# Kernel tuning notes

Measured on AMD Instinct MI355X. Metric: run time of the kernel, lower is better.

Reference implementation:

```python
import jax, jax.numpy as jnp
import numpy as np
from jax.scipy.linalg import solve_triangular

L_SUB = 16          # subarray length (init arg L)
DL = 0.05           # diagonal loading factor


def setup_inputs() -> dict:
    key = jax.random.key(0)
    k0, k1, k2 = jax.random.split(key, 3)
    B, C, NS, NZ, NX = 2, 128, 1024, 256, 128
    rf = jax.random.normal(k0, (B, C, NS), jnp.float32)
    t0 = jnp.zeros((B,), jnp.float32)
    d_tx = jax.random.uniform(k1, (B, NZ, NX), dtype=jnp.float32)
    d_rx = jax.random.uniform(k2, (C, NZ, NX), dtype=jnp.float32)
    fs = jnp.float32((NS - 1) / 2.0)   # keeps sample positions in [0, NS-1]
    f0 = jnp.float32(5.0)              # unused by forward (kept for signature parity)
    c0 = jnp.float32(1.0)
    apod = jnp.ones((C,), jnp.float32) # unused by forward
    return dict(rf=rf, t0=t0, d_tx=d_tx, d_rx=d_rx, fs=fs, f0=f0, c0=c0, apod=apod)


def _aligned_signals(rf, t0, d_tx, d_rx, fs, c0):
    """Bilinear (1-D linear) resample of rf at per-pixel delays.
    Equivalent to torch grid_sample(mode='bilinear', padding_mode='border',
    align_corners=True) where the grid x-coord is samples*2/(NS-1)-1."""
    B, C, NS = rf.shape
    _, NZ, NX = d_tx.shape
    # samples: [B, C, NZ, NX] fractional sample index into rf
    samples = fs * ((d_tx[:, None, :, :] + d_rx[None, :, :, :]) / c0
                    + t0[:, None, None, None])
    pos = jnp.clip(samples, 0.0, NS - 1.0)          # border padding
    i0 = jnp.floor(pos).astype(jnp.int32)
    i1 = jnp.minimum(i0 + 1, NS - 1)
    frac = pos - i0.astype(pos.dtype)
    sig = rf.reshape(B * C, NS)
    i0f = i0.reshape(B * C, NZ * NX)
    i1f = i1.reshape(B * C, NZ * NX)
    v0 = jnp.take_along_axis(sig, i0f, axis=1).reshape(B, C, NZ, NX)
    v1 = jnp.take_along_axis(sig, i1f, axis=1).reshape(B, C, NZ, NX)
    return v0 * (1.0 - frac) + v1 * frac


def reference(rf, t0, d_tx, d_rx, fs, f0, c0, apod):
    B, C, NS = rf.shape
    _, NZ, NX = d_tx.shape
    M = C - L_SUB + 1  # number of subarrays (113)
    aligned = _aligned_signals(rf, t0, d_tx, d_rx, fs, c0)  # [B, C, NZ, NX]
    # per-pixel channel vectors: [P, C], P = B*NZ*NX
    xf = aligned.transpose(0, 2, 3, 1).reshape(-1, C)
    # subarray gather: S[p, m, l] = xf[p, m + l]  -> [P, M, L]
    idx = jnp.arange(M)[:, None] + jnp.arange(L_SUB)[None, :]
    S = xf[:, idx]
    # avg_pool1d(kernel=M, stride=1) over channels == mean over subarray axis
    x = S.mean(axis=1)                                  # [P, L]
    # spatially-smoothed covariance: R = S^T S / M, symmetrized
    R = jnp.einsum('pml,pmk->plk', S, S) / M
    R = 0.5 * (R + R.transpose(0, 2, 1))
    # diagonal loading: R += dl * (trace/L) * I
    delta = jnp.trace(R, axis1=-2, axis2=-1) / L_SUB    # [P]
    R = R + (DL * delta)[:, None, None] * jnp.eye(L_SUB, dtype=R.dtype)
    # Cholesky solve R u = 1
    Lc = jnp.linalg.cholesky(R)
    rhs = jnp.ones((R.shape[0], L_SUB, 1), R.dtype)
    y1 = solve_triangular(Lc, rhs, lower=True)
    u = solve_triangular(Lc, y1, lower=True, trans=1)[..., 0]  # [P, L]
    # MVDR weights (steering a = ones) and beamformed output
    denom = jnp.sum(u, axis=-1, keepdims=True) + 1e-10
    w = u / denom
    y = jnp.sum(w * x, axis=-1)                         # [P]
    return y.reshape(B, NZ, NX)
```

## Files before the change

### kernel.cpp

```cpp
#include <hip/hip_runtime.h>


namespace {

constexpr int kB  = 2;
constexpr int kC  = 128;
constexpr int kNS = 1024;
constexpr int kNZ = 256;
constexpr int kNX = 128;
constexpr int kZX = kNZ * kNX;
constexpr int kNPIX = kB * kZX;
constexpr int kChunk = 8;
constexpr int kChunkF = kChunk * kNS;
constexpr int kTPA = 256;

__device__ __host__ constexpr int tri(int l, int k) {
  return l * 16 - (l * (l - 1)) / 2 + (k - l);
}

typedef __attribute__((address_space(1))) const void gconst_t;
typedef __attribute__((address_space(3))) void ldsv_t;

__device__ __forceinline__ void g2l16(const float* g, float* l) {
  __builtin_amdgcn_global_load_lds((gconst_t*)g, (ldsv_t*)l, 16, 0, 0);
}

__device__ __forceinline__ void stage_chunk(const float* __restrict__ gsrc,
                                            float* ldst, int woff, int lane) {
#pragma unroll
  for (int i = 0; i < 8; ++i)
    g2l16(gsrc + woff + i * 256 + lane * 4, ldst + woff + i * 256);
}

__device__ __forceinline__ void load_drx(const float* __restrict__ drx_px,
                                         int cbase, float (&d)[kChunk]) {
#pragma unroll
  for (int r = 0; r < kChunk; ++r)
    d[r] = drx_px[(size_t)(cbase + r) * kZX];
}

template <int PH, bool HEAD>
__device__ __forceinline__ void chunk_compute(
    const float* rows, const float (&drx)[kChunk], float kk, float base,
    float (&F)[16], float (&win)[16], float (&head)[16], float& Sall) {
#pragma unroll
  for (int r = 0; r < kChunk; ++r) {
    const int t = PH + r;
    float pos = fmaf(kk, drx[r], base);
    pos = fminf(fmaxf(pos, 0.0f), 1023.0f);
    int i0 = (int)pos;
    i0 = min(i0, kNS - 2);
    float frac = pos - (float)i0;
    const float* p = rows + r * kNS + i0;
    float v0 = p[0];
    float v1 = p[1];
    float v = fmaf(frac, v1 - v0, v0);
    Sall += v;
    F[0] = fmaf(v, v, F[0]);
    if constexpr (HEAD) {
#pragma unroll
      for (int d = 1; d <= t; ++d) F[d] = fmaf(v, win[t - d], F[d]);
      head[t] = v;
    } else {
#pragma unroll
      for (int d = 1; d < 16; ++d) F[d] = fmaf(v, win[(t - d) & 15], F[d]);
    }
    win[t] = v;
  }
}

__global__ __launch_bounds__(kTPA, 1) void mvb_window_kernel(
    const float* __restrict__ rf, const float* __restrict__ t0,
    const float* __restrict__ d_tx, const float* __restrict__ d_rx,
    const float* __restrict__ fs_p, const float* __restrict__ c0_p,
    float* __restrict__ ws) {
  __shared__ float tile[2 * kChunkF];

  const int tid = threadIdx.x;
  const int lane = tid & 63;
  const int wave = tid >> 6;
  const int woff = wave * 2048;
  const int b = blockIdx.x >> 7;
  const int z = ((blockIdx.x & 127) << 1) + (tid >> 7);
  const int x = tid & 127;
  const int pix = (int)((size_t)b * kZX + z * kNX + x);

  const float fs = fs_p[0];
  const float c0 = c0_p[0];
  const float kk = fs / c0;
  const float base = fs * (d_tx[pix] / c0 + t0[b]);

  const float* rfb = rf + (size_t)b * kC * kNS;
  const float* drx_px = d_rx + (size_t)z * kNX + x;

  float F[16], win[16], head[16];
  float Sall = 0.0f;
#pragma unroll
  for (int i = 0; i < 16; ++i) F[i] = 0.0f;

  float drx0[kChunk], drx1[kChunk];

  stage_chunk(rfb, tile, woff, lane);
  load_drx(drx_px, 0, drx0);
  __syncthreads();

  stage_chunk(rfb + kChunkF, tile + kChunkF, woff, lane);
  load_drx(drx_px, 8, drx1);
  chunk_compute<0, true>(tile, drx0, kk, base, F, win, head, Sall);
  __syncthreads();

  stage_chunk(rfb + 2 * kChunkF, tile, woff, lane);
  load_drx(drx_px, 16, drx0);
  chunk_compute<8, true>(tile + kChunkF, drx1, kk, base, F, win, head, Sall);
  __syncthreads();

  for (int g = 0; g < 7; ++g) {
    const int q0 = 2 * g + 2;
    stage_chunk(rfb + (size_t)(q0 + 1) * kChunkF, tile + kChunkF, woff, lane);
    load_drx(drx_px, (q0 + 1) * kChunk, drx1);
    chunk_compute<0, false>(tile, drx0, kk, base, F, win, head, Sall);
    __syncthreads();

    if (q0 + 2 < 16) {
      stage_chunk(rfb + (size_t)(q0 + 2) * kChunkF, tile, woff, lane);
      load_drx(drx_px, (q0 + 2) * kChunk, drx0);
    }
    chunk_compute<8, false>(tile + kChunkF, drx1, kk, base, F, win, head,
                            Sall);
    __syncthreads();
  }

#pragma unroll
  for (int i = 0; i < 16; ++i) ws[(size_t)i * kNPIX + pix] = F[i];
#pragma unroll
  for (int i = 0; i < 16; ++i) ws[(size_t)(16 + i) * kNPIX + pix] = win[i];
#pragma unroll
  for (int i = 0; i < 16; ++i) ws[(size_t)(32 + i) * kNPIX + pix] = head[i];
  ws[(size_t)48 * kNPIX + pix] = Sall;
}

__global__ __launch_bounds__(64, 1) void mvb_solve_kernel(
    const float* __restrict__ ws, float* __restrict__ out) {
  const int pix = blockIdx.x * 64 + threadIdx.x;

  float F[16], win[16], head[16];
#pragma unroll
  for (int i = 0; i < 16; ++i) F[i] = ws[(size_t)i * kNPIX + pix];
#pragma unroll
  for (int i = 0; i < 16; ++i) win[i] = ws[(size_t)(16 + i) * kNPIX + pix];
#pragma unroll
  for (int i = 0; i < 16; ++i) head[i] = ws[(size_t)(32 + i) * kNPIX + pix];
  const float Sall = ws[(size_t)48 * kNPIX + pix];

  float Ru[136];
#pragma unroll
  for (int d = 0; d < 16; ++d) {
    float t0s = 0.0f;
#pragma unroll
    for (int i = d + 1; i < 16; ++i) t0s = fmaf(win[i - d], win[i], t0s);
    Ru[tri(0, d)] = F[d] - t0s;
#pragma unroll
    for (int l = 1; l < 16 - d; ++l)
      Ru[tri(l, l + d)] = Ru[tri(l - 1, l - 1 + d)] -
                          head[l - 1] * head[l - 1 + d] +
                          win[l] * win[l + d];
  }

  float tr = 0.0f;
#pragma unroll
  for (int l = 0; l < 16; ++l) tr += Ru[tri(l, l)];
  const float dl = tr * (0.05f / 16.0f);
#pragma unroll
  for (int l = 0; l < 16; ++l) Ru[tri(l, l)] += dl;

  float X[16];
  {
    float s = Sall;
#pragma unroll
    for (int i = 1; i < 16; ++i) s -= win[i];
    X[0] = s;
#pragma unroll
    for (int l = 1; l < 16; ++l) X[l] = X[l - 1] - head[l - 1] + win[l];
  }

  float inv[16];
#pragma unroll
  for (int j = 0; j < 16; ++j) {
    float d = Ru[tri(j, j)];
#pragma unroll
    for (int p = 0; p < j; ++p) d = fmaf(-Ru[tri(p, j)], Ru[tri(p, j)], d);
    float Ljj = sqrtf(d);
    inv[j] = 1.0f / Ljj;
    Ru[tri(j, j)] = Ljj;
#pragma unroll
    for (int i = j + 1; i < 16; ++i) {
      float s = Ru[tri(j, i)];
#pragma unroll
      for (int p = 0; p < j; ++p) s = fmaf(-Ru[tri(p, i)], Ru[tri(p, j)], s);
      Ru[tri(j, i)] = s * inv[j];
    }
  }

  float yv[16];
#pragma unroll
  for (int i = 0; i < 16; ++i) {
    float s = 1.0f;
#pragma unroll
    for (int j = 0; j < i; ++j) s = fmaf(-Ru[tri(j, i)], yv[j], s);
    yv[i] = s * inv[i];
  }
  float u[16];
#pragma unroll
  for (int i = 15; i >= 0; --i) {
    float s = yv[i];
#pragma unroll
    for (int j = i + 1; j < 16; ++j) s = fmaf(-Ru[tri(i, j)], u[j], s);
    u[i] = s * inv[i];
  }

  float su = 0.0f, dot = 0.0f;
#pragma unroll
  for (int i = 0; i < 16; ++i) {
    su += u[i];
    dot = fmaf(u[i], X[i], dot);
  }
  out[pix] = dot / (113.0f * su + 1e-10f);
}

}

extern "C" void kernel_launch(void* const* d_in, const int* in_sizes, int n_in,
                              void* d_out, int out_size, void* d_ws,
                              size_t ws_size, hipStream_t stream) {
  const float* rf   = (const float*)d_in[0];
  const float* t0   = (const float*)d_in[1];
  const float* d_tx = (const float*)d_in[2];
  const float* d_rx = (const float*)d_in[3];
  const float* fs   = (const float*)d_in[4];
  const float* c0   = (const float*)d_in[6];
  float* out = (float*)d_out;
  float* ws  = (float*)d_ws;

  hipLaunchKernelGGL(mvb_window_kernel, dim3(kB * kNZ / 2), dim3(kTPA), 0,
                     stream, rf, t0, d_tx, d_rx, fs, c0, ws);
  hipLaunchKernelGGL(mvb_solve_kernel, dim3(kNPIX / 64), dim3(64), 0, stream,
                     ws, out);
}
```

Before: 100.2 us.

## Fuse window accumulation and Cholesky solve into one kernel with 128-thread blocks

Merges the window-statistics kernel and the per-pixel Cholesky solve kernel into a single kernel, removing the 49-float-per-pixel workspace round trip through global memory and one kernel launch. Blocks shrink from 256 to 128 threads (one z row each), so each wave now stages twice as much of the rf chunk into LDS, and the grid doubles to 512 blocks. The Cholesky diagonal uses rsqrtf directly instead of sqrt plus reciprocal. The risk is higher register pressure in the fused kernel, since it holds both accumulators and the 136-entry triangle, together with fewer threads per block sharing each LDS tile, so more staging work per thread.

```diff
diff --git a/kernel.cpp b/kernel.cpp
--- a/kernel.cpp
+++ b/kernel.cpp
@@ -9,10 +9,9 @@
 constexpr int kNZ = 256;
 constexpr int kNX = 128;
 constexpr int kZX = kNZ * kNX;
-constexpr int kNPIX = kB * kZX;
 constexpr int kChunk = 8;
 constexpr int kChunkF = kChunk * kNS;
-constexpr int kTPA = 256;
+constexpr int kTPB = 128;
 
 __device__ __host__ constexpr int tri(int l, int k) {
   return l * 16 - (l * (l - 1)) / 2 + (k - l);
@@ -28,7 +27,7 @@
 __device__ __forceinline__ void stage_chunk(const float* __restrict__ gsrc,
                                             float* ldst, int woff, int lane) {
 #pragma unroll
-  for (int i = 0; i < 8; ++i)
+  for (int i = 0; i < 16; ++i)
     g2l16(gsrc + woff + i * 256 + lane * 4, ldst + woff + i * 256);
 }
 
@@ -69,20 +68,20 @@
   }
 }
 
-__global__ __launch_bounds__(kTPA, 1) void mvb_window_kernel(
+__global__ __launch_bounds__(kTPB, 1) void mvb_fused_kernel(
     const float* __restrict__ rf, const float* __restrict__ t0,
     const float* __restrict__ d_tx, const float* __restrict__ d_rx,
     const float* __restrict__ fs_p, const float* __restrict__ c0_p,
-    float* __restrict__ ws) {
+    float* __restrict__ out) {
   __shared__ float tile[2 * kChunkF];
 
   const int tid = threadIdx.x;
   const int lane = tid & 63;
   const int wave = tid >> 6;
-  const int woff = wave * 2048;
-  const int b = blockIdx.x >> 7;
-  const int z = ((blockIdx.x & 127) << 1) + (tid >> 7);
-  const int x = tid & 127;
+  const int woff = wave * 4096;
+  const int z = blockIdx.x & (kNZ - 1);
+  const int b = blockIdx.x >> 8;
+  const int x = tid;
   const int pix = (int)((size_t)b * kZX + z * kNX + x);
 
   const float fs = fs_p[0];
@@ -130,28 +129,6 @@
     __syncthreads();
   }
 
-#pragma unroll
-  for (int i = 0; i < 16; ++i) ws[(size_t)i * kNPIX + pix] = F[i];
-#pragma unroll
-  for (int i = 0; i < 16; ++i) ws[(size_t)(16 + i) * kNPIX + pix] = win[i];
-#pragma unroll
-  for (int i = 0; i < 16; ++i) ws[(size_t)(32 + i) * kNPIX + pix] = head[i];
-  ws[(size_t)48 * kNPIX + pix] = Sall;
-}
-
-__global__ __launch_bounds__(64, 1) void mvb_solve_kernel(
-    const float* __restrict__ ws, float* __restrict__ out) {
-  const int pix = blockIdx.x * 64 + threadIdx.x;
-
-  float F[16], win[16], head[16];
-#pragma unroll
-  for (int i = 0; i < 16; ++i) F[i] = ws[(size_t)i * kNPIX + pix];
-#pragma unroll
-  for (int i = 0; i < 16; ++i) win[i] = ws[(size_t)(16 + i) * kNPIX + pix];
-#pragma unroll
-  for (int i = 0; i < 16; ++i) head[i] = ws[(size_t)(32 + i) * kNPIX + pix];
-  const float Sall = ws[(size_t)48 * kNPIX + pix];
-
   float Ru[136];
 #pragma unroll
   for (int d = 0; d < 16; ++d) {
@@ -189,9 +166,7 @@
     float d = Ru[tri(j, j)];
 #pragma unroll
     for (int p = 0; p < j; ++p) d = fmaf(-Ru[tri(p, j)], Ru[tri(p, j)], d);
-    float Ljj = sqrtf(d);
-    inv[j] = 1.0f / Ljj;
-    Ru[tri(j, j)] = Ljj;
+    inv[j] = rsqrtf(d);
 #pragma unroll
     for (int i = j + 1; i < 16; ++i) {
       float s = Ru[tri(j, i)];
@@ -239,10 +214,7 @@
   const float* fs   = (const float*)d_in[4];
   const float* c0   = (const float*)d_in[6];
   float* out = (float*)d_out;
-  float* ws  = (float*)d_ws;
-
-  hipLaunchKernelGGL(mvb_window_kernel, dim3(kB * kNZ / 2), dim3(kTPA), 0,
-                     stream, rf, t0, d_tx, d_rx, fs, c0, ws);
-  hipLaunchKernelGGL(mvb_solve_kernel, dim3(kNPIX / 64), dim3(64), 0, stream,
-                     ws, out);
-}
+
+  hipLaunchKernelGGL(mvb_fused_kernel, dim3(kB * kNZ), dim3(kTPB), 0, stream,
+                     rf, t0, d_tx, d_rx, fs, c0, out);
+}
```

Result: faster. 95.44 us (-4.7%).
